# Kernel tuning notes

Measured on AMD Instinct MI355X. Metric: run time of the kernel, lower is better.

The kernel has to match this reference:

```python
import jax, jax.numpy as jnp
import numpy as np

TEMPERATURE = 0.05
EPS = 1e-6
N, D = 8192, 64


def setup_inputs() -> dict:
    key = jax.random.key(0)
    k1, k2 = jax.random.split(key)
    anchor_embeddings = jax.random.normal(k1, (N, D), dtype=jnp.float32)
    positive_embeddings = jax.random.normal(k2, (N, D), dtype=jnp.float32)
    return {"anchor_embeddings": anchor_embeddings,
            "positive_embeddings": positive_embeddings}


def _cos_matrix(x, y, nx, ny):
    # pairwise cosine sim with torch CosineSimilarity eps semantics:
    # dot / max(||x||*||y||, eps)
    return (x @ y.T) / jnp.maximum(nx[:, None] * ny[None, :], EPS)


def reference(anchor_embeddings, positive_embeddings):
    a, p = anchor_embeddings, positive_embeddings
    na = jnp.linalg.norm(a, axis=-1)  # [N]
    npn = jnp.linalg.norm(p, axis=-1)  # [N]

    inv_t = 1.0 / TEMPERATURE
    S_ap = _cos_matrix(a, p, na, npn)  # [N, N]
    S_aa = _cos_matrix(a, a, na, na)   # [N, N]
    S_pp = _cos_matrix(p, p, npn, npn)  # [N, N]

    E_ap = jnp.exp(S_ap * inv_t)
    E_aa = jnp.exp(S_aa * inv_t)
    E_pp = jnp.exp(S_pp * inv_t)

    self_term = jnp.exp(jnp.asarray(inv_t, dtype=a.dtype))  # exp(1/T)
    # partition_i = sum_j E_ap[i,j] + sum_j E_aa[i,j] - e^{1/T}
    #             + sum_j E_ap[j,i] + sum_j E_pp[j,i] - e^{1/T}
    partition = (E_ap.sum(axis=1) + E_aa.sum(axis=1)
                 + E_ap.sum(axis=0) + E_pp.sum(axis=0)
                 - 2.0 * self_term)

    # loss = -mean_i log( exp(cos(a_i,p_i)/T) / partition_i )
    pos_logit = jnp.diagonal(S_ap) * inv_t
    loss = -jnp.mean(pos_logit - jnp.log(partition))
    return loss
```

## Files before the change

kernel.cpp:

```cpp
#include <hip/hip_runtime.h>
#include <hip/hip_bf16.h>
#include <math.h>

#define N 8192
#define D 64
#define INVT 20.0f
#define EPS 1e-6f
#define ZSCALE 5.3715835f

typedef __attribute__((ext_vector_type(8))) short bf16x8;
typedef __attribute__((ext_vector_type(4))) float f32x4;

#if __has_builtin(__builtin_amdgcn_exp2f)
#define EXP2F(x) __builtin_amdgcn_exp2f(x)
#else
#define EXP2F(x) exp2f(x)
#endif


__global__ __launch_bounds__(256) void prep_kernel(
    const float* __restrict__ A, const float* __restrict__ P,
    __hip_bfloat16* __restrict__ Zn, float* __restrict__ diag20,
    float* __restrict__ part, float* __restrict__ lacc, unsigned* __restrict__ cnt) {
    if (blockIdx.x < 64) part[blockIdx.x * 256 + threadIdx.x] = 0.0f;
    else if (blockIdx.x == 64 && threadIdx.x == 0) { *lacc = 0.0f; *cnt = 0u; }

    const int lane = threadIdx.x & 63;
    const int w    = threadIdx.x >> 6;
    const int r    = blockIdx.x * 4 + w;
    const int u    = lane >> 3, sub = lane & 7;
    const int upos = (u >> 2) * 64 + (u & 3) * 16;

    float a = A[r * D + lane];
    float p = P[r * D + lane];
    float sa = a * a, sp = p * p, dp = a * p;
    #pragma unroll
    for (int off = 1; off < 64; off <<= 1) {
        sa += __shfl_xor(sa, off, 64);
        sp += __shfl_xor(sp, off, 64);
        dp += __shfl_xor(dp, off, 64);
    }
    float na  = sqrtf(sa);
    float npn = sqrtf(sp);
    {
        int g = r >> 4, l2 = r & 15;
        Zn[(g * 128 + upos + l2) * 8 + sub] = __float2bfloat16(a * (ZSCALE / na));
    }
    {
        int R = N + r; int g = R >> 4, l2 = R & 15;
        Zn[(g * 128 + upos + l2) * 8 + sub] = __float2bfloat16(p * (ZSCALE / npn));
    }
    if (lane == 0)
        diag20[r] = (dp / fmaxf(na * npn, EPS)) * INVT;
}

__global__ __launch_bounds__(256, 4) void tiles_kernel(
    const __hip_bfloat16* __restrict__ Zn, float* __restrict__ part) {
    __shared__ float rs[4][16][68];
    __shared__ float merged[2][128];
    __shared__ float cmerged[2][2][64];

    int t = (int)blockIdx.x;
    int b = (int)((257.0f - sqrtf(66049.0f - 8.0f * (float)t)) * 0.5f);
    while (b * (257 - b) / 2 > t) --b;
    while ((b + 1) * (256 - b) / 2 <= t) ++b;
    const int bi = b;
    const int bj = b + (t - b * (257 - b) / 2);
    const bool diag = (bi == bj);

    const int tid = threadIdx.x;
    const int lane = tid & 63, w = tid >> 6;
    const int wr = w >> 1, wc = w & 1;
    const int ln = lane & 15, q = lane >> 4;
    const bf16x8* Zf = (const bf16x8*)Zn;

    bf16x8 af[4][2], bv[4][2];
    #pragma unroll
    for (int ii = 0; ii < 4; ++ii) {
        int ga = bi * 8 + wr * 4 + ii;
        int gb = bj * 8 + wc * 4 + ii;
        #pragma unroll
        for (int kc = 0; kc < 2; ++kc) {
            af[ii][kc] = Zf[ga * 128 + kc * 64 + lane];
            bv[ii][kc] = Zf[gb * 128 + kc * 64 + lane];
        }
    }

    const bool dwave = diag && (wr == wc);
    const f32x4 zero = {0.0f, 0.0f, 0.0f, 0.0f};
    f32x4 csumv[4] = {};

    #pragma unroll
    for (int ii = 0; ii < 4; ++ii) {
        f32x4 acc[4];
        #pragma unroll
        for (int jj = 0; jj < 4; ++jj)
            acc[jj] = __builtin_amdgcn_mfma_f32_16x16x32_bf16(
                af[ii][0], bv[jj][0], zero, 0, 0, 0);
        #pragma unroll
        for (int jj = 0; jj < 4; ++jj)
            acc[jj] = __builtin_amdgcn_mfma_f32_16x16x32_bf16(
                af[ii][1], bv[jj][1], acc[jj], 0, 0, 0);

        f32x4 rsum_ii = {};
        #pragma unroll
        for (int jj = 0; jj < 4; ++jj) {
            f32x4 e;
            #pragma unroll
            for (int r = 0; r < 4; ++r) e[r] = EXP2F(acc[jj][r]);
            if (dwave && (ii == jj)) {
                #pragma unroll
                for (int r = 0; r < 4; ++r)
                    if (ln == q * 4 + r) e[r] = 0.0f;
            }
            rsum_ii += e;
            csumv[jj] += e;
        }
        *(f32x4*)&rs[w][ln][ii * 16 + q * 4] = rsum_ii;
    }

    float rowsum = 0.0f;
    #pragma unroll
    for (int l = 0; l < 16; ++l) rowsum += rs[w][l][lane];
    merged[wc][wr * 64 + lane] = rowsum;

    float cs0 = (csumv[0][0] + csumv[0][1]) + (csumv[0][2] + csumv[0][3]);
    float cs1 = (csumv[1][0] + csumv[1][1]) + (csumv[1][2] + csumv[1][3]);
    float cs2 = (csumv[2][0] + csumv[2][1]) + (csumv[2][2] + csumv[2][3]);
    float cs3 = (csumv[3][0] + csumv[3][1]) + (csumv[3][2] + csumv[3][3]);
    cs0 += __shfl_xor(cs0, 16, 64); cs0 += __shfl_xor(cs0, 32, 64);
    cs1 += __shfl_xor(cs1, 16, 64); cs1 += __shfl_xor(cs1, 32, 64);
    cs2 += __shfl_xor(cs2, 16, 64); cs2 += __shfl_xor(cs2, 32, 64);
    cs3 += __shfl_xor(cs3, 16, 64); cs3 += __shfl_xor(cs3, 32, 64);
    float cval = (q == 0) ? cs0 : (q == 1) ? cs1 : (q == 2) ? cs2 : cs3;
    cmerged[wr][wc][q * 16 + ln] = cval;
    __syncthreads();

    if (tid < 128) {
        atomicAdd(part + bi * 128 + tid, merged[0][tid] + merged[1][tid]);
    } else if (!diag) {
        int col = tid - 128;
        atomicAdd(part + bj * 128 + col,
                  cmerged[0][col >> 6][col & 63] + cmerged[1][col >> 6][col & 63]);
    }
}

__global__ __launch_bounds__(256) void loss_kernel(
    const float* __restrict__ part, const float* __restrict__ diag20,
    float* __restrict__ lacc, unsigned* __restrict__ cnt, float* __restrict__ out) {
    int i = blockIdx.x * 256 + threadIdx.x;
    float v = logf(part[i] + part[N + i]) - diag20[i];
    #pragma unroll
    for (int off = 32; off > 0; off >>= 1) v += __shfl_down(v, off, 64);
    __shared__ float wsm[4];
    int lane = threadIdx.x & 63, wv = threadIdx.x >> 6;
    if (lane == 0) wsm[wv] = v;
    __syncthreads();
    if (threadIdx.x == 0) {
        atomicAdd(lacc, wsm[0] + wsm[1] + wsm[2] + wsm[3]);
        __threadfence();
        unsigned old = atomicAdd(cnt, 1u);
        if (old == (N / 256 - 1)) {
            float tot = atomicAdd(lacc, 0.0f);
            out[0] = tot * (1.0f / (float)N);
        }
    }
}

extern "C" void kernel_launch(void* const* d_in, const int* in_sizes, int n_in,
                              void* d_out, int out_size, void* d_ws, size_t ws_size,
                              hipStream_t stream) {
    const float* A = (const float*)d_in[0];
    const float* P = (const float*)d_in[1];

    __hip_bfloat16* Zn = (__hip_bfloat16*)d_ws;
    float* diag20 = (float*)((char*)d_ws + 2u * N * D * sizeof(__hip_bfloat16));
    float* part   = diag20 + N;
    float* lacc   = part + 2 * N;
    unsigned* cnt = (unsigned*)(lacc + 1);

    prep_kernel<<<N / 4, 256, 0, stream>>>(A, P, Zn, diag20, part, lacc, cnt);

    const int nblocks = 128 * 129 / 2;
    tiles_kernel<<<nblocks, 256, 0, stream>>>(Zn, part);

    loss_kernel<<<N / 256, 256, 0, stream>>>(part, diag20, lacc, cnt, (float*)d_out);
}
```

Baseline: 93.09 us.

## Fuse loss reduction into tiles kernel via last-block counter and stream A fragments

Removes the separate loss kernel launch. The last tiles block, found with an atomic counter, now computes the log-partition loss over all rows. A-operand fragments are loaded one row-group at a time with prefetch of the next, and column sums are reduced to scalars early. Together these cut register pressure so launch bounds can rise from 4 to 5 blocks per CU. The cost is a serial tail where a single block reduces 8192 rows, plus an extra syncthreads and atomic in every block.

```diff
diff --git a/kernel.cpp b/kernel.cpp
--- a/kernel.cpp
+++ b/kernel.cpp
@@ -7,6 +7,7 @@
 #define INVT 20.0f
 #define EPS 1e-6f
 #define ZSCALE 5.3715835f
+#define NBLOCKS (128 * 129 / 2)
 
 typedef __attribute__((ext_vector_type(8))) short bf16x8;
 typedef __attribute__((ext_vector_type(4))) float f32x4;
@@ -54,11 +55,15 @@
         diag20[r] = (dp / fmaxf(na * npn, EPS)) * INVT;
 }
 
-__global__ __launch_bounds__(256, 4) void tiles_kernel(
-    const __hip_bfloat16* __restrict__ Zn, float* __restrict__ part) {
+__global__ __launch_bounds__(256, 5) void tiles_kernel(
+    const __hip_bfloat16* __restrict__ Zn, float* __restrict__ part,
+    const float* __restrict__ diag20, unsigned* __restrict__ cnt,
+    float* __restrict__ out) {
     __shared__ float rs[4][16][68];
     __shared__ float merged[2][128];
     __shared__ float cmerged[2][2][64];
+    __shared__ int   last_flag;
+    __shared__ float wsm[4];
 
     int t = (int)blockIdx.x;
     int b = (int)((257.0f - sqrtf(66049.0f - 8.0f * (float)t)) * 0.5f);
@@ -74,33 +79,39 @@
     const int ln = lane & 15, q = lane >> 4;
     const bf16x8* Zf = (const bf16x8*)Zn;
 
-    bf16x8 af[4][2], bv[4][2];
+    bf16x8 bv[4][2];
     #pragma unroll
-    for (int ii = 0; ii < 4; ++ii) {
-        int ga = bi * 8 + wr * 4 + ii;
-        int gb = bj * 8 + wc * 4 + ii;
+    for (int jj = 0; jj < 4; ++jj) {
+        int gb = bj * 8 + wc * 4 + jj;
         #pragma unroll
-        for (int kc = 0; kc < 2; ++kc) {
-            af[ii][kc] = Zf[ga * 128 + kc * 64 + lane];
-            bv[ii][kc] = Zf[gb * 128 + kc * 64 + lane];
-        }
+        for (int kc = 0; kc < 2; ++kc)
+            bv[jj][kc] = Zf[gb * 128 + kc * 64 + lane];
     }
+
+    const int gaBase = (bi * 8 + wr * 4) * 128 + lane;
+    bf16x8 afc0 = Zf[gaBase];
+    bf16x8 afc1 = Zf[gaBase + 64];
 
     const bool dwave = diag && (wr == wc);
     const f32x4 zero = {0.0f, 0.0f, 0.0f, 0.0f};
-    f32x4 csumv[4] = {};
+    float csum[4] = {0.0f, 0.0f, 0.0f, 0.0f};
 
     #pragma unroll
     for (int ii = 0; ii < 4; ++ii) {
+        bf16x8 afn0, afn1;
+        if (ii < 3) {
+            afn0 = Zf[gaBase + (ii + 1) * 128];
+            afn1 = Zf[gaBase + (ii + 1) * 128 + 64];
+        }
         f32x4 acc[4];
         #pragma unroll
         for (int jj = 0; jj < 4; ++jj)
             acc[jj] = __builtin_amdgcn_mfma_f32_16x16x32_bf16(
-                af[ii][0], bv[jj][0], zero, 0, 0, 0);
+                afc0, bv[jj][0], zero, 0, 0, 0);
         #pragma unroll
         for (int jj = 0; jj < 4; ++jj)
             acc[jj] = __builtin_amdgcn_mfma_f32_16x16x32_bf16(
-                af[ii][1], bv[jj][1], acc[jj], 0, 0, 0);
+                afc1, bv[jj][1], acc[jj], 0, 0, 0);
 
         f32x4 rsum_ii = {};
         #pragma unroll
@@ -114,9 +125,10 @@
                     if (ln == q * 4 + r) e[r] = 0.0f;
             }
             rsum_ii += e;
-            csumv[jj] += e;
+            csum[jj] += (e[0] + e[1]) + (e[2] + e[3]);
         }
         *(f32x4*)&rs[w][ln][ii * 16 + q * 4] = rsum_ii;
+        afc0 = afn0; afc1 = afn1;
     }
 
     float rowsum = 0.0f;
@@ -124,10 +136,7 @@
     for (int l = 0; l < 16; ++l) rowsum += rs[w][l][lane];
     merged[wc][wr * 64 + lane] = rowsum;
 
-    float cs0 = (csumv[0][0] + csumv[0][1]) + (csumv[0][2] + csumv[0][3]);
-    float cs1 = (csumv[1][0] + csumv[1][1]) + (csumv[1][2] + csumv[1][3]);
-    float cs2 = (csumv[2][0] + csumv[2][1]) + (csumv[2][2] + csumv[2][3]);
-    float cs3 = (csumv[3][0] + csumv[3][1]) + (csumv[3][2] + csumv[3][3]);
+    float cs0 = csum[0], cs1 = csum[1], cs2 = csum[2], cs3 = csum[3];
     cs0 += __shfl_xor(cs0, 16, 64); cs0 += __shfl_xor(cs0, 32, 64);
     cs1 += __shfl_xor(cs1, 16, 64); cs1 += __shfl_xor(cs1, 32, 64);
     cs2 += __shfl_xor(cs2, 16, 64); cs2 += __shfl_xor(cs2, 32, 64);
@@ -143,27 +152,26 @@
         atomicAdd(part + bj * 128 + col,
                   cmerged[0][col >> 6][col & 63] + cmerged[1][col >> 6][col & 63]);
     }
-}
 
-__global__ __launch_bounds__(256) void loss_kernel(
-    const float* __restrict__ part, const float* __restrict__ diag20,
-    float* __restrict__ lacc, unsigned* __restrict__ cnt, float* __restrict__ out) {
-    int i = blockIdx.x * 256 + threadIdx.x;
-    float v = logf(part[i] + part[N + i]) - diag20[i];
-    #pragma unroll
-    for (int off = 32; off > 0; off >>= 1) v += __shfl_down(v, off, 64);
-    __shared__ float wsm[4];
-    int lane = threadIdx.x & 63, wv = threadIdx.x >> 6;
-    if (lane == 0) wsm[wv] = v;
     __syncthreads();
-    if (threadIdx.x == 0) {
-        atomicAdd(lacc, wsm[0] + wsm[1] + wsm[2] + wsm[3]);
+    if (tid == 0) {
         __threadfence();
         unsigned old = atomicAdd(cnt, 1u);
-        if (old == (N / 256 - 1)) {
-            float tot = atomicAdd(lacc, 0.0f);
-            out[0] = tot * (1.0f / (float)N);
-        }
+        last_flag = (old == NBLOCKS - 1) ? 1 : 0;
+    }
+    __syncthreads();
+    if (last_flag) {
+        __threadfence();
+        float v = 0.0f;
+        #pragma unroll 4
+        for (int i = tid; i < N; i += 256)
+            v += logf(part[i] + part[N + i]) - diag20[i];
+        #pragma unroll
+        for (int off = 32; off > 0; off >>= 1) v += __shfl_down(v, off, 64);
+        if (lane == 0) wsm[w] = v;
+        __syncthreads();
+        if (tid == 0)
+            out[0] = (wsm[0] + wsm[1] + wsm[2] + wsm[3]) * (1.0f / (float)N);
     }
 }
 
@@ -181,8 +189,5 @@
 
     prep_kernel<<<N / 4, 256, 0, stream>>>(A, P, Zn, diag20, part, lacc, cnt);
 
-    const int nblocks = 128 * 129 / 2;
-    tiles_kernel<<<nblocks, 256, 0, stream>>>(Zn, part);
-
-    loss_kernel<<<N / 256, 256, 0, stream>>>(part, diag20, lacc, cnt, (float*)d_out);
+    tiles_kernel<<<NBLOCKS, 256, 0, stream>>>(Zn, part, diag20, cnt, (float*)d_out);
 }
```

New measurement: 330.6 us. +255.1%, slower.

## Process two triangle tiles per block and prefetch the second tile's operands

Applied to the files above, without the earlier changes.

Each block of the tiles kernel now handles two consecutive upper-triangle tiles, which halves the grid size. The second tile's bf16 fragments are loaded while the first tile's row and column sums are reduced and atomically added, so global load latency overlaps with the reduction. Column partial sums are also reduced to scalars inside the loop instead of being kept as vectors. The cost is extra live registers under launch bounds of (256,4), with some risk of spilling or lower occupancy, plus fewer blocks for load balancing.

```diff
diff --git a/kernel.cpp b/kernel.cpp
--- a/kernel.cpp
+++ b/kernel.cpp
@@ -17,6 +17,14 @@
 #define EXP2F(x) exp2f(x)
 #endif
 
+
+__device__ __forceinline__ void unrank(int t, int& bi, int& bj) {
+    int b = (int)((257.0f - sqrtf(66049.0f - 8.0f * (float)t)) * 0.5f);
+    while (b * (257 - b) / 2 > t) --b;
+    while ((b + 1) * (256 - b) / 2 <= t) ++b;
+    bi = b;
+    bj = b + (t - b * (257 - b) / 2);
+}
 
 __global__ __launch_bounds__(256) void prep_kernel(
     const float* __restrict__ A, const float* __restrict__ P,
@@ -60,47 +68,43 @@
     __shared__ float merged[2][128];
     __shared__ float cmerged[2][2][64];
 
-    int t = (int)blockIdx.x;
-    int b = (int)((257.0f - sqrtf(66049.0f - 8.0f * (float)t)) * 0.5f);
-    while (b * (257 - b) / 2 > t) --b;
-    while ((b + 1) * (256 - b) / 2 <= t) ++b;
-    const int bi = b;
-    const int bj = b + (t - b * (257 - b) / 2);
-    const bool diag = (bi == bj);
-
     const int tid = threadIdx.x;
     const int lane = tid & 63, w = tid >> 6;
     const int wr = w >> 1, wc = w & 1;
     const int ln = lane & 15, q = lane >> 4;
     const bf16x8* Zf = (const bf16x8*)Zn;
 
-    bf16x8 af[4][2], bv[4][2];
-    #pragma unroll
-    for (int ii = 0; ii < 4; ++ii) {
-        int ga = bi * 8 + wr * 4 + ii;
-        int gb = bj * 8 + wc * 4 + ii;
+    int bi0, bj0, bi1, bj1;
+    unrank(2 * (int)blockIdx.x,     bi0, bj0);
+    unrank(2 * (int)blockIdx.x + 1, bi1, bj1);
+
+    const f32x4 zero = {0.0f, 0.0f, 0.0f, 0.0f};
+
+    bf16x8 af0[4][2], bv0[4][2];
+    #pragma unroll
+    for (int ii = 0; ii < 4; ++ii) {
+        int ga = bi0 * 8 + wr * 4 + ii;
+        int gb = bj0 * 8 + wc * 4 + ii;
         #pragma unroll
         for (int kc = 0; kc < 2; ++kc) {
-            af[ii][kc] = Zf[ga * 128 + kc * 64 + lane];
-            bv[ii][kc] = Zf[gb * 128 + kc * 64 + lane];
-        }
-    }
-
-    const bool dwave = diag && (wr == wc);
-    const f32x4 zero = {0.0f, 0.0f, 0.0f, 0.0f};
-    f32x4 csumv[4] = {};
-
+            af0[ii][kc] = Zf[ga * 128 + kc * 64 + lane];
+            bv0[ii][kc] = Zf[gb * 128 + kc * 64 + lane];
+        }
+    }
+
+    const bool dwave0 = (bi0 == bj0) && (wr == wc);
+    float csum[4] = {0.0f, 0.0f, 0.0f, 0.0f};
     #pragma unroll
     for (int ii = 0; ii < 4; ++ii) {
         f32x4 acc[4];
         #pragma unroll
         for (int jj = 0; jj < 4; ++jj)
             acc[jj] = __builtin_amdgcn_mfma_f32_16x16x32_bf16(
-                af[ii][0], bv[jj][0], zero, 0, 0, 0);
-        #pragma unroll
-        for (int jj = 0; jj < 4; ++jj)
-            acc[jj] = __builtin_amdgcn_mfma_f32_16x16x32_bf16(
-                af[ii][1], bv[jj][1], acc[jj], 0, 0, 0);
+                af0[ii][0], bv0[jj][0], zero, 0, 0, 0);
+        #pragma unroll
+        for (int jj = 0; jj < 4; ++jj)
+            acc[jj] = __builtin_amdgcn_mfma_f32_16x16x32_bf16(
+                af0[ii][1], bv0[jj][1], acc[jj], 0, 0, 0);
 
         f32x4 rsum_ii = {};
         #pragma unroll
@@ -108,40 +112,107 @@
             f32x4 e;
             #pragma unroll
             for (int r = 0; r < 4; ++r) e[r] = EXP2F(acc[jj][r]);
-            if (dwave && (ii == jj)) {
+            if (dwave0 && (ii == jj)) {
                 #pragma unroll
                 for (int r = 0; r < 4; ++r)
                     if (ln == q * 4 + r) e[r] = 0.0f;
             }
             rsum_ii += e;
-            csumv[jj] += e;
+            csum[jj] += (e[0] + e[1]) + (e[2] + e[3]);
         }
         *(f32x4*)&rs[w][ln][ii * 16 + q * 4] = rsum_ii;
     }
 
-    float rowsum = 0.0f;
-    #pragma unroll
-    for (int l = 0; l < 16; ++l) rowsum += rs[w][l][lane];
-    merged[wc][wr * 64 + lane] = rowsum;
-
-    float cs0 = (csumv[0][0] + csumv[0][1]) + (csumv[0][2] + csumv[0][3]);
-    float cs1 = (csumv[1][0] + csumv[1][1]) + (csumv[1][2] + csumv[1][3]);
-    float cs2 = (csumv[2][0] + csumv[2][1]) + (csumv[2][2] + csumv[2][3]);
-    float cs3 = (csumv[3][0] + csumv[3][1]) + (csumv[3][2] + csumv[3][3]);
-    cs0 += __shfl_xor(cs0, 16, 64); cs0 += __shfl_xor(cs0, 32, 64);
-    cs1 += __shfl_xor(cs1, 16, 64); cs1 += __shfl_xor(cs1, 32, 64);
-    cs2 += __shfl_xor(cs2, 16, 64); cs2 += __shfl_xor(cs2, 32, 64);
-    cs3 += __shfl_xor(cs3, 16, 64); cs3 += __shfl_xor(cs3, 32, 64);
-    float cval = (q == 0) ? cs0 : (q == 1) ? cs1 : (q == 2) ? cs2 : cs3;
-    cmerged[wr][wc][q * 16 + ln] = cval;
+    bf16x8 af1[4][2], bv1[4][2];
+    #pragma unroll
+    for (int ii = 0; ii < 4; ++ii) {
+        int ga = bi1 * 8 + wr * 4 + ii;
+        int gb = bj1 * 8 + wc * 4 + ii;
+        #pragma unroll
+        for (int kc = 0; kc < 2; ++kc) {
+            af1[ii][kc] = Zf[ga * 128 + kc * 64 + lane];
+            bv1[ii][kc] = Zf[gb * 128 + kc * 64 + lane];
+        }
+    }
+
+    {
+        float rowsum = 0.0f;
+        #pragma unroll
+        for (int l = 0; l < 16; ++l) rowsum += rs[w][l][lane];
+        merged[wc][wr * 64 + lane] = rowsum;
+
+        float cs0 = csum[0], cs1 = csum[1], cs2 = csum[2], cs3 = csum[3];
+        cs0 += __shfl_xor(cs0, 16, 64); cs0 += __shfl_xor(cs0, 32, 64);
+        cs1 += __shfl_xor(cs1, 16, 64); cs1 += __shfl_xor(cs1, 32, 64);
+        cs2 += __shfl_xor(cs2, 16, 64); cs2 += __shfl_xor(cs2, 32, 64);
+        cs3 += __shfl_xor(cs3, 16, 64); cs3 += __shfl_xor(cs3, 32, 64);
+        float cval = (q == 0) ? cs0 : (q == 1) ? cs1 : (q == 2) ? cs2 : cs3;
+        cmerged[wr][wc][q * 16 + ln] = cval;
+        __syncthreads();
+
+        if (tid < 128) {
+            atomicAdd(part + bi0 * 128 + tid, merged[0][tid] + merged[1][tid]);
+        } else if (bi0 != bj0) {
+            int col = tid - 128;
+            atomicAdd(part + bj0 * 128 + col,
+                      cmerged[0][col >> 6][col & 63] + cmerged[1][col >> 6][col & 63]);
+        }
+    }
     __syncthreads();
 
-    if (tid < 128) {
-        atomicAdd(part + bi * 128 + tid, merged[0][tid] + merged[1][tid]);
-    } else if (!diag) {
-        int col = tid - 128;
-        atomicAdd(part + bj * 128 + col,
-                  cmerged[0][col >> 6][col & 63] + cmerged[1][col >> 6][col & 63]);
+    const bool dwave1 = (bi1 == bj1) && (wr == wc);
+    float csumB[4] = {0.0f, 0.0f, 0.0f, 0.0f};
+    #pragma unroll
+    for (int ii = 0; ii < 4; ++ii) {
+        f32x4 acc[4];
+        #pragma unroll
+        for (int jj = 0; jj < 4; ++jj)
+            acc[jj] = __builtin_amdgcn_mfma_f32_16x16x32_bf16(
+                af1[ii][0], bv1[jj][0], zero, 0, 0, 0);
+        #pragma unroll
+        for (int jj = 0; jj < 4; ++jj)
+            acc[jj] = __builtin_amdgcn_mfma_f32_16x16x32_bf16(
+                af1[ii][1], bv1[jj][1], acc[jj], 0, 0, 0);
+
+        f32x4 rsum_ii = {};
+        #pragma unroll
+        for (int jj = 0; jj < 4; ++jj) {
+            f32x4 e;
+            #pragma unroll
+            for (int r = 0; r < 4; ++r) e[r] = EXP2F(acc[jj][r]);
+            if (dwave1 && (ii == jj)) {
+                #pragma unroll
+                for (int r = 0; r < 4; ++r)
+                    if (ln == q * 4 + r) e[r] = 0.0f;
+            }
+            rsum_ii += e;
+            csumB[jj] += (e[0] + e[1]) + (e[2] + e[3]);
+        }
+        *(f32x4*)&rs[w][ln][ii * 16 + q * 4] = rsum_ii;
+    }
+
+    {
+        float rowsum = 0.0f;
+        #pragma unroll
+        for (int l = 0; l < 16; ++l) rowsum += rs[w][l][lane];
+        merged[wc][wr * 64 + lane] = rowsum;
+
+        float cs0 = csumB[0], cs1 = csumB[1], cs2 = csumB[2], cs3 = csumB[3];
+        cs0 += __shfl_xor(cs0, 16, 64); cs0 += __shfl_xor(cs0, 32, 64);
+        cs1 += __shfl_xor(cs1, 16, 64); cs1 += __shfl_xor(cs1, 32, 64);
+        cs2 += __shfl_xor(cs2, 16, 64); cs2 += __shfl_xor(cs2, 32, 64);
+        cs3 += __shfl_xor(cs3, 16, 64); cs3 += __shfl_xor(cs3, 32, 64);
+        float cval = (q == 0) ? cs0 : (q == 1) ? cs1 : (q == 2) ? cs2 : cs3;
+        cmerged[wr][wc][q * 16 + ln] = cval;
+        __syncthreads();
+
+        if (tid < 128) {
+            atomicAdd(part + bi1 * 128 + tid, merged[0][tid] + merged[1][tid]);
+        } else if (bi1 != bj1) {
+            int col = tid - 128;
+            atomicAdd(part + bj1 * 128 + col,
+                      cmerged[0][col >> 6][col & 63] + cmerged[1][col >> 6][col & 63]);
+        }
     }
 }
 
@@ -181,7 +252,7 @@
 
     prep_kernel<<<N / 4, 256, 0, stream>>>(A, P, Zn, diag20, part, lacc, cnt);
 
-    const int nblocks = 128 * 129 / 2;
+    const int nblocks = 128 * 129 / 4;
     tiles_kernel<<<nblocks, 256, 0, stream>>>(Zn, part);
 
     loss_kernel<<<N / 256, 256, 0, stream>>>(part, diag20, lacc, cnt, (float*)d_out);
```

After: 92.93 us, median of 2. Within noise of the previous version (-0.2%).
